# Kernel tuning notes

Measured on AMD Instinct MI355X. Metric: run time of the kernel, lower is better.

The kernel has to match this reference:

```python
import jax, jax.numpy as jnp
import numpy as np

B, IN, O, F, FH = 512, 2000, 64, 8, 32
D = 64 + FH * O  # 2112


def setup_inputs() -> dict:
    key = jax.random.key(0)
    ks = jax.random.split(key, 17)
    rn = lambda k, s: jax.random.normal(k, s, dtype=jnp.float32) * 0.05
    return dict(
        x=rn(ks[0], (B, IN)),
        fc_in_W=rn(ks[1], (1024, IN)), fc_in_b=rn(ks[2], (1024,)),
        fc1_W=rn(ks[3], (128, 1024)), fc1_b=rn(ks[4], (128,)),
        out1_W=rn(ks[5], (O, 64, 128)), out1_b=rn(ks[6], (O, 64)),
        coef_nn_W=rn(ks[7], (F, FH, 1)), coef_nn_b=rn(ks[8], (F, FH)),
        coef_att_W=rn(ks[9], (F, FH, FH)),
        out_att_W=rn(ks[10], (O, FH, FH)),
        nodes_trans_W=rn(ks[11], (O, O)),
        trans_gcn_W=rn(ks[12], (D, D)),
        outmap_W=rn(ks[13], (1, D)), outmap_b=rn(ks[14], (1,)),
        prelu_a=jnp.float32(0.25),
        coef_m=rn(ks[15], (O, O, F)),
    )


def reference(x, fc_in_W, fc_in_b, fc1_W, fc1_b, out1_W, out1_b,
              coef_nn_W, coef_nn_b, coef_att_W, out_att_W,
              nodes_trans_W, trans_gcn_W, outmap_W, outmap_b, prelu_a, coef_m):
    elu = jax.nn.elu
    # trunk MLP
    h = jax.nn.relu(x @ fc_in_W.T + fc_in_b)          # [B,1024]
    h = jax.nn.relu(h @ fc1_W.T + fc1_b)              # [B,128]
    # per-output-node heads (vectorized over the output_dim loop)
    hiddens = jax.nn.relu(jnp.einsum('bk,odk->bod', h, out1_W) + out1_b)  # [B,O,64]
    # per-feature coef embedding: Linear(1,FH) on each coef_m[:,:,i] slice
    cf = elu(coef_m[..., None] * coef_nn_W[:, :, 0] + coef_nn_b)          # [O,O,F,FH]
    # sum over concatenated feature axis (F*FH) of exp(elu(.))
    s = jnp.exp(elu(cf)).sum(axis=(2, 3))[:, :, None, None]               # [O,O,1,1]
    lin = jnp.einsum('xyfh,fgh->xyfg', cf, coef_att_W)                    # per-feature attention linear
    p = elu(jnp.exp(elu(cf)) * lin / s)
    cfs = elu(p.sum(axis=2) / F)                                          # [O,O,FH]
    # node-level attention (vectorized over the output_dim loop)
    coef_sum = jnp.exp(elu(cfs)).sum(axis=1)                              # [O,FH]
    p2 = jnp.exp(elu(cfs)) / coef_sum[:, None, :]                         # [O,O,FH]
    lin2 = jnp.einsum('oih,igh->oig', cfs, out_att_W)
    att = (p2 * lin2).reshape(O, O * FH)                                  # concat over i (i-major)
    hc = jnp.concatenate(
        [hiddens, jnp.broadcast_to(att[None], (x.shape[0], O, O * FH))], axis=2)  # [B,O,D]
    nt = jnp.einsum('bpd,op->bod', hc, nodes_trans_W)                     # node mixing Linear(O,O)
    trans = jax.nn.sigmoid(jnp.einsum('bod,ed->boe', nt, trans_gcn_W))    # [B,O,D]
    z = (trans @ outmap_W.T + outmap_b).squeeze(-1)                       # [B,O]
    return jnp.where(z >= 0, z, prelu_a * z)                              # PReLU
```

## Files before the change

kernel.cpp:

```cpp
#include <hip/hip_runtime.h>
#include <math.h>

typedef __attribute__((ext_vector_type(8))) short bf16x8;
typedef __attribute__((ext_vector_type(4))) float f32x4;

static __device__ __forceinline__ float fast_elu(float x) {
    return x > 0.0f ? x : __expf(x) - 1.0f;
}

static __device__ __forceinline__ unsigned short f2bf(float f) {
    unsigned int u = __float_as_uint(f);
    unsigned int r = (u + 0x7FFFu + ((u >> 16) & 1u)) >> 16;
    return (unsigned short)r;
}

#define CV0 1048576
#define CV1 3145728
#define CV2 3276800
#define CV3 3280896
#define CV4 3805184
#define CV5 8265728
__global__ __launch_bounds__(256) void conv_all(
    const float* __restrict__ x, const float* __restrict__ fcinW,
    const float* __restrict__ fc1W, const float* __restrict__ ntW,
    const float* __restrict__ out1W, const float* __restrict__ tgw,
    unsigned short* __restrict__ xb, unsigned short* __restrict__ fcinWb,
    unsigned short* __restrict__ fc1Wb, unsigned short* __restrict__ Wb,
    unsigned short* __restrict__ out1WbT,
    unsigned short* __restrict__ Gb, unsigned short* __restrict__ G2b)
{
    int idx = blockIdx.x * 256 + threadIdx.x;
    if (idx < CV0) {
        int r = idx >> 11, k = idx & 2047;
        xb[idx] = (k < 2000) ? f2bf(x[(size_t)r * 2000 + k]) : (unsigned short)0;
    } else if (idx < CV1) {
        int i = idx - CV0;
        int r = i >> 11, k = i & 2047;
        fcinWb[i] = (k < 2000) ? f2bf(fcinW[(size_t)r * 2000 + k]) : (unsigned short)0;
    } else if (idx < CV2) {
        int i = idx - CV1;
        fc1Wb[i] = f2bf(fc1W[i]);
    } else if (idx < CV3) {
        int i = idx - CV2;
        Wb[i] = f2bf(ntW[i]);
    } else if (idx < CV4) {
        int i = idx - CV3;
        int n = i >> 7, k = i & 127, d = n >> 6, p = n & 63;
        out1WbT[i] = f2bf(out1W[(size_t)((p << 6) | d) * 128 + k]);
    } else if (idx < CV5) {
        int i = idx - CV4;
        int e = i / 2112, k = i - e * 2112;
        unsigned short v = f2bf(tgw[(size_t)e * 2112 + k]);
        if (k < 64) Gb[e * 64 + k] = v;
        else        G2b[(size_t)e * 2048 + (k - 64)] = v;
    }
}

__global__ __launch_bounds__(256) void gemm_mfma(
    const unsigned short* __restrict__ A, int lda,
    const unsigned short* __restrict__ B, int ldb,
    float* __restrict__ C, unsigned short* __restrict__ Cb,
    int ldc, long strideCz,
    const float* __restrict__ bias, int mode, int kchunk)
{
    __shared__ __align__(16) unsigned short As[64 * 40];
    __shared__ __align__(16) unsigned short Bs[64 * 40];
    const int t = threadIdx.x;
    const int w = t >> 6, lane = t & 63, l16 = lane & 15, quad = lane >> 4;
    const int n0 = blockIdx.x * 64, m0 = blockIdx.y * 64;
    const int kb0 = blockIdx.z * kchunk;
    const int r = t >> 2, koff = (t & 3) * 8;
    if (mode == 0) C += (size_t)blockIdx.z * strideCz;

    const size_t arow = (size_t)(m0 + r) * lda + koff;
    const size_t brow = (size_t)(n0 + r) * ldb + koff;
    bf16x8 av = *reinterpret_cast<const bf16x8*>(&A[arow + kb0]);
    bf16x8 bv = *reinterpret_cast<const bf16x8*>(&B[brow + kb0]);

    f32x4 acc[4] = {};
    for (int kb = kb0; kb < kb0 + kchunk; kb += 32) {
        __syncthreads();
        *reinterpret_cast<bf16x8*>(&As[r * 40 + koff]) = av;
        *reinterpret_cast<bf16x8*>(&Bs[r * 40 + koff]) = bv;
        if (kb + 32 < kb0 + kchunk) {
            av = *reinterpret_cast<const bf16x8*>(&A[arow + kb + 32]);
            bv = *reinterpret_cast<const bf16x8*>(&B[brow + kb + 32]);
        }
        __syncthreads();
        bf16x8 af = *reinterpret_cast<const bf16x8*>(&As[(w * 16 + l16) * 40 + quad * 8]);
        #pragma unroll
        for (int nt = 0; nt < 4; ++nt) {
            bf16x8 bf = *reinterpret_cast<const bf16x8*>(&Bs[(nt * 16 + l16) * 40 + quad * 8]);
            acc[nt] = __builtin_amdgcn_mfma_f32_16x16x32_bf16(af, bf, acc[nt], 0, 0, 0);
        }
    }
    #pragma unroll
    for (int nt = 0; nt < 4; ++nt)
        #pragma unroll
        for (int i = 0; i < 4; ++i) {
            int m = m0 + w * 16 + quad * 4 + i;
            int n = n0 + nt * 16 + l16;
            if (mode == 0) {
                C[(size_t)m * ldc + n] = acc[nt][i];
            } else {
                int bidx = (((n & 63) << 6) | (n >> 6));
                float v = acc[nt][i] + bias[bidx];
                v = fmaxf(v, 0.0f);
                Cb[(size_t)m * ldc + n] = f2bf(v);
            }
        }
}

__global__ __launch_bounds__(256) void gemm_mfma_fa(
    const float* __restrict__ Ap, int lda, long apstride, int nparts,
    const float* __restrict__ abias,
    const unsigned short* __restrict__ B, int ldb,
    float* __restrict__ C, unsigned short* __restrict__ Cb,
    int ldc, long strideCz,
    const float* __restrict__ bias, int mode, int kchunk)
{
    __shared__ __align__(16) unsigned short As[64 * 40];
    __shared__ __align__(16) unsigned short Bs[64 * 40];
    const int t = threadIdx.x;
    const int w = t >> 6, lane = t & 63, l16 = lane & 15, quad = lane >> 4;
    const int n0 = blockIdx.x * 64, m0 = blockIdx.y * 64;
    const int kb0 = blockIdx.z * kchunk;
    const int r = t >> 2, koff = (t & 3) * 8;
    if (mode == 0) C += (size_t)blockIdx.z * strideCz;

    f32x4 acc[4] = {};
    for (int kb = kb0; kb < kb0 + kchunk; kb += 32) {
        float a8[8];
        {
            const float* base = &Ap[(size_t)(m0 + r) * lda + kb + koff];
            float4 s0 = *reinterpret_cast<const float4*>(base);
            float4 s1 = *reinterpret_cast<const float4*>(base + 4);
            for (int j = 1; j < nparts; ++j) {
                const float* pj = base + (size_t)j * apstride;
                float4 p0 = *reinterpret_cast<const float4*>(pj);
                float4 p1 = *reinterpret_cast<const float4*>(pj + 4);
                s0.x += p0.x; s0.y += p0.y; s0.z += p0.z; s0.w += p0.w;
                s1.x += p1.x; s1.y += p1.y; s1.z += p1.z; s1.w += p1.w;
            }
            float4 b0 = *reinterpret_cast<const float4*>(&abias[kb + koff]);
            float4 b1 = *reinterpret_cast<const float4*>(&abias[kb + koff + 4]);
            a8[0] = fmaxf(s0.x + b0.x, 0.0f); a8[1] = fmaxf(s0.y + b0.y, 0.0f);
            a8[2] = fmaxf(s0.z + b0.z, 0.0f); a8[3] = fmaxf(s0.w + b0.w, 0.0f);
            a8[4] = fmaxf(s1.x + b1.x, 0.0f); a8[5] = fmaxf(s1.y + b1.y, 0.0f);
            a8[6] = fmaxf(s1.z + b1.z, 0.0f); a8[7] = fmaxf(s1.w + b1.w, 0.0f);
        }
        bf16x8 bv = *reinterpret_cast<const bf16x8*>(&B[(size_t)(n0 + r) * ldb + kb + koff]);
        __syncthreads();
        ushort4 lo, hi;
        lo.x = f2bf(a8[0]); lo.y = f2bf(a8[1]); lo.z = f2bf(a8[2]); lo.w = f2bf(a8[3]);
        hi.x = f2bf(a8[4]); hi.y = f2bf(a8[5]); hi.z = f2bf(a8[6]); hi.w = f2bf(a8[7]);
        *reinterpret_cast<ushort4*>(&As[r * 40 + koff]) = lo;
        *reinterpret_cast<ushort4*>(&As[r * 40 + koff + 4]) = hi;
        *reinterpret_cast<bf16x8*>(&Bs[r * 40 + koff]) = bv;
        __syncthreads();
        bf16x8 af = *reinterpret_cast<const bf16x8*>(&As[(w * 16 + l16) * 40 + quad * 8]);
        #pragma unroll
        for (int nt = 0; nt < 4; ++nt) {
            bf16x8 bf = *reinterpret_cast<const bf16x8*>(&Bs[(nt * 16 + l16) * 40 + quad * 8]);
            acc[nt] = __builtin_amdgcn_mfma_f32_16x16x32_bf16(af, bf, acc[nt], 0, 0, 0);
        }
    }
    #pragma unroll
    for (int nt = 0; nt < 4; ++nt)
        #pragma unroll
        for (int i = 0; i < 4; ++i) {
            int m = m0 + w * 16 + quad * 4 + i;
            int n = n0 + nt * 16 + l16;
            if (mode == 0) {
                C[(size_t)m * ldc + n] = acc[nt][i];
            } else {
                int bidx = (((n & 63) << 6) | (n >> 6));
                float v = acc[nt][i] + bias[bidx];
                v = fmaxf(v, 0.0f);
                Cb[(size_t)m * ldc + n] = f2bf(v);
            }
        }
}

__global__ __launch_bounds__(256) void reduce_partials(
    const float* __restrict__ src, float* __restrict__ dst, int n,
    int nparts, long pstride)
{
    int i = blockIdx.x * 256 + threadIdx.x;
    if (i >= n) return;
    float a = 0.0f;
    for (int j = 0; j < nparts; ++j) a += src[i + (long)j * pstride];
    dst[i] = a;
}

__global__ __launch_bounds__(256) void coef_kernel(
    const float* __restrict__ coef_m,
    const float* __restrict__ cW,
    const float* __restrict__ cB,
    const float* __restrict__ attW,
    float* __restrict__ cfs)
{
    __shared__ float cf_s[4][256];
    __shared__ float part[4][64];
    const int t = threadIdx.x;
    const int wv = t >> 6, lane = t & 63;
    const int xy = blockIdx.x * 4 + wv;
    float ls = 0.0f;
    #pragma unroll
    for (int i = 0; i < 4; ++i) {
        int idx = i * 64 + lane;
        int f = idx >> 5;
        float v = fast_elu(coef_m[xy * 8 + f] * cW[idx] + cB[idx]);
        cf_s[wv][idx] = v;
        ls += __expf(fast_elu(v));
    }
    #pragma unroll
    for (int m = 1; m < 64; m <<= 1) ls += __shfl_xor(ls, m, 64);
    __syncthreads();
    const float rs = __builtin_amdgcn_rcpf(ls);
    const int g = lane & 31, fg = lane >> 5;
    float acc = 0.0f;
    for (int f = fg * 4; f < fg * 4 + 4; ++f) {
        float lin = 0.0f;
        #pragma unroll
        for (int h = 0; h < 32; h += 4) {
            float4 Lv = *reinterpret_cast<const float4*>(&cf_s[wv][f * 32 + h]);
            float4 Wv = *reinterpret_cast<const float4*>(&attW[f * 1024 + g * 32 + h]);
            lin += Lv.x * Wv.x + Lv.y * Wv.y + Lv.z * Wv.z + Lv.w * Wv.w;
        }
        float e = __expf(fast_elu(cf_s[wv][f * 32 + g]));
        acc += fast_elu(e * lin * rs);
    }
    part[wv][lane] = acc;
    __syncthreads();
    if (lane < 32) {
        float tot = part[wv][lane] + part[wv][lane + 32];
        cfs[xy * 32 + lane] = fast_elu(tot * 0.125f);
    }
}

__global__ __launch_bounds__(256) void att_split(
    const float* __restrict__ cfs,
    const float* __restrict__ oattW,
    float* __restrict__ att)
{
    __shared__ float L[2048];
    __shared__ float red[256];
    __shared__ float csum[32];
    const int t = threadIdx.x;
    const int o = blockIdx.x;
    const int ic = blockIdx.y;
    #pragma unroll
    for (int j = 0; j < 8; ++j) L[t + 256 * j] = cfs[o * 2048 + t + 256 * j];
    __syncthreads();
    {
        int h = t & 31, ig = t >> 5;
        float ps = 0.0f;
        for (int i = ig * 8; i < ig * 8 + 8; ++i) ps += __expf(fast_elu(L[i * 32 + h]));
        red[t] = ps;
        __syncthreads();
        if (t < 32) {
            float cs = 0.0f;
            #pragma unroll
            for (int j = 0; j < 8; ++j) cs += red[j * 32 + t];
            csum[t] = cs;
        }
        __syncthreads();
    }
    int idx = ic * 256 + t;
    int i = idx >> 5, g = idx & 31;
    float lin2 = 0.0f;
    #pragma unroll
    for (int h = 0; h < 32; h += 4) {
        float4 Lv = *reinterpret_cast<const float4*>(&L[i * 32 + h]);
        float4 Wv = *reinterpret_cast<const float4*>(&oattW[i * 1024 + g * 32 + h]);
        lin2 += Lv.x * Wv.x + Lv.y * Wv.y + Lv.z * Wv.z + Lv.w * Wv.w;
    }
    float p2 = __expf(fast_elu(L[idx])) * __builtin_amdgcn_rcpf(csum[g]);
    att[o * 2048 + idx] = p2 * lin2;
}

__global__ __launch_bounds__(256) void natt_new(
    const float* __restrict__ ntW,
    const float* __restrict__ att,
    unsigned short* __restrict__ nattb)
{
    __shared__ float ntW_s[64 * 65];
    __shared__ float att_s[64 * 17];
    const int t = threadIdx.x;
    const int d0 = blockIdx.x * 16;
    #pragma unroll
    for (int j = 0; j < 16; ++j) {
        int idx = t + 256 * j;
        ntW_s[(idx >> 6) * 65 + (idx & 63)] = ntW[idx];
    }
    #pragma unroll
    for (int j = 0; j < 4; ++j) {
        int idx = t + 256 * j;
        int p = idx >> 4, dd = idx & 15;
        att_s[p * 17 + dd] = att[p * 2048 + d0 + dd];
    }
    __syncthreads();
    const int dd = t & 15, ob = (t >> 4) * 4;
    float acc[4] = {0.0f, 0.0f, 0.0f, 0.0f};
    for (int p = 0; p < 64; ++p) {
        float av = att_s[p * 17 + dd];
        #pragma unroll
        for (int i = 0; i < 4; ++i) acc[i] += ntW_s[(ob + i) * 65 + p] * av;
    }
    #pragma unroll
    for (int i = 0; i < 4; ++i)
        nattb[(ob + i) * 2048 + d0 + dd] = f2bf(acc[i]);
}

__global__ __launch_bounds__(256) void nt1f(
    const unsigned short* __restrict__ hbT,
    const unsigned short* __restrict__ Wb,
    unsigned short* __restrict__ nt1b)
{
    __shared__ __align__(16) unsigned short HtT[64 * 72];
    __shared__ __align__(16) unsigned short nt1_s[64 * 72];
    const int t = threadIdx.x;
    const int w = t >> 6, lane = t & 63, l16 = lane & 15, quad = lane >> 4;
    const int b = blockIdx.x;

    const unsigned short* src = hbT + (size_t)b * 4096;
    #pragma unroll
    for (int j = 0; j < 2; ++j) {
        int c = t + j * 256;
        *reinterpret_cast<bf16x8*>(&HtT[(c >> 3) * 72 + (c & 7) * 8]) =
            *reinterpret_cast<const bf16x8*>(&src[c * 8]);
    }
    __syncthreads();

    bf16x8 aW[2];
    #pragma unroll
    for (int h = 0; h < 2; ++h)
        aW[h] = *reinterpret_cast<const bf16x8*>(&Wb[(w * 16 + l16) * 64 + h * 32 + quad * 8]);
    #pragma unroll
    for (int dt = 0; dt < 4; ++dt) {
        f32x4 acc = {0.0f, 0.0f, 0.0f, 0.0f};
        #pragma unroll
        for (int h = 0; h < 2; ++h) {
            bf16x8 bf = *reinterpret_cast<const bf16x8*>(
                &HtT[(dt * 16 + l16) * 72 + h * 32 + quad * 8]);
            acc = __builtin_amdgcn_mfma_f32_16x16x32_bf16(aW[h], bf, acc, 0, 0, 0);
        }
        #pragma unroll
        for (int i = 0; i < 4; ++i)
            nt1_s[(w * 16 + quad * 4 + i) * 72 + dt * 16 + l16] = f2bf(acc[i]);
    }
    __syncthreads();
    #pragma unroll
    for (int j = 0; j < 2; ++j) {
        int c = t + j * 256;
        *reinterpret_cast<bf16x8*>(&nt1b[(size_t)b * 4096 + c * 8]) =
            *reinterpret_cast<const bf16x8*>(&nt1_s[(c >> 3) * 72 + (c & 7) * 8]);
    }
}

__global__ __launch_bounds__(256) void final_eblk(
    const unsigned short* __restrict__ nt1b,
    const unsigned short* __restrict__ Gb,
    const float* __restrict__ cmatT,
    const float* __restrict__ outW,
    float* __restrict__ zpart)
{
    __shared__ __align__(16) unsigned short nls[2][64 * 72];
    __shared__ float zs[2][4][64];
    const int t = threadIdx.x;
    const int w = t >> 6, lane = t & 63, l16 = lane & 15, quad = lane >> 4;
    const int eb = blockIdx.x;
    const int b0 = blockIdx.y * 32;
    const int ew = eb * 64 + w * 16;

    bf16x8 ga[2];
    #pragma unroll
    for (int h = 0; h < 2; ++h)
        ga[h] = *reinterpret_cast<const bf16x8*>(
            &Gb[(size_t)(ew + l16) * 64 + h * 32 + quad * 8]);
    float cm[4][4];
    #pragma unroll
    for (int nt = 0; nt < 4; ++nt)
        #pragma unroll
        for (int i = 0; i < 4; ++i)
            cm[nt][i] = cmatT[(size_t)(ew + quad * 4 + i) * 64 + nt * 16 + l16];
    float wv[4];
    #pragma unroll
    for (int i = 0; i < 4; ++i) wv[i] = outW[ew + quad * 4 + i];

    const int c0 = t, c1 = t + 256;
    bf16x8 v0 = *reinterpret_cast<const bf16x8*>(&nt1b[(size_t)b0 * 4096 + c0 * 8]);
    bf16x8 v1 = *reinterpret_cast<const bf16x8*>(&nt1b[(size_t)b0 * 4096 + c1 * 8]);
    *reinterpret_cast<bf16x8*>(&nls[0][(c0 >> 3) * 72 + (c0 & 7) * 8]) = v0;
    *reinterpret_cast<bf16x8*>(&nls[0][(c1 >> 3) * 72 + (c1 & 7) * 8]) = v1;
    __syncthreads();

    int cur = 0;
    for (int bi = 0; bi < 32; ++bi) {
        if (bi < 31) {
            v0 = *reinterpret_cast<const bf16x8*>(
                &nt1b[(size_t)(b0 + bi + 1) * 4096 + c0 * 8]);
            v1 = *reinterpret_cast<const bf16x8*>(
                &nt1b[(size_t)(b0 + bi + 1) * 4096 + c1 * 8]);
        }
        if (bi > 0 && t < 64) {
            const float* z = &zs[(bi - 1) & 1][0][0];
            zpart[((size_t)eb * 512 + b0 + bi - 1) * 64 + t] =
                z[t] + z[64 + t] + z[128 + t] + z[192 + t];
        }
        float zo[4] = {0.0f, 0.0f, 0.0f, 0.0f};
        #pragma unroll
        for (int nt = 0; nt < 4; ++nt) {
            bf16x8 bf0 = *reinterpret_cast<const bf16x8*>(
                &nls[cur][(nt * 16 + l16) * 72 + quad * 8]);
            bf16x8 bf1 = *reinterpret_cast<const bf16x8*>(
                &nls[cur][(nt * 16 + l16) * 72 + 32 + quad * 8]);
            f32x4 acc = {cm[nt][0], cm[nt][1], cm[nt][2], cm[nt][3]};
            acc = __builtin_amdgcn_mfma_f32_16x16x32_bf16(ga[0], bf0, acc, 0, 0, 0);
            acc = __builtin_amdgcn_mfma_f32_16x16x32_bf16(ga[1], bf1, acc, 0, 0, 0);
            #pragma unroll
            for (int i = 0; i < 4; ++i)
                zo[nt] += __builtin_amdgcn_rcpf(1.0f + __expf(-acc[i])) * wv[i];
        }
        #pragma unroll
        for (int nt = 0; nt < 4; ++nt) {
            zo[nt] += __shfl_xor(zo[nt], 16, 64);
            zo[nt] += __shfl_xor(zo[nt], 32, 64);
        }
        if (quad == 0) {
            #pragma unroll
            for (int nt = 0; nt < 4; ++nt)
                zs[bi & 1][w][nt * 16 + l16] = zo[nt];
        }
        if (bi < 31) {
            *reinterpret_cast<bf16x8*>(&nls[1 - cur][(c0 >> 3) * 72 + (c0 & 7) * 8]) = v0;
            *reinterpret_cast<bf16x8*>(&nls[1 - cur][(c1 >> 3) * 72 + (c1 & 7) * 8]) = v1;
        }
        __syncthreads();
        cur ^= 1;
    }
    if (t < 64) {
        const float* z = &zs[1][0][0];
        zpart[((size_t)eb * 512 + b0 + 31) * 64 + t] =
            z[t] + z[64 + t] + z[128 + t] + z[192 + t];
    }
}

__global__ __launch_bounds__(256) void finish_kernel(
    const float* __restrict__ zpart, const float* __restrict__ outB,
    const float* __restrict__ preluA, float* __restrict__ out)
{
    int i = blockIdx.x * 256 + threadIdx.x;
    float z = 0.0f;
    for (int j = 0; j < 33; ++j) z += zpart[(size_t)j * 32768 + i];
    z += outB[0];
    float pa = preluA[0];
    out[i] = (z >= 0.0f) ? z : pa * z;
}

extern "C" void kernel_launch(void* const* d_in, const int* in_sizes, int n_in,
                              void* d_out, int out_size, void* d_ws, size_t ws_size,
                              hipStream_t stream)
{
    const float* x       = (const float*)d_in[0];
    const float* fc_in_W = (const float*)d_in[1];
    const float* fc_in_b = (const float*)d_in[2];
    const float* fc1_W   = (const float*)d_in[3];
    const float* fc1_b   = (const float*)d_in[4];
    const float* out1_W  = (const float*)d_in[5];
    const float* out1_b  = (const float*)d_in[6];
    const float* cW      = (const float*)d_in[7];
    const float* cB      = (const float*)d_in[8];
    const float* cattW   = (const float*)d_in[9];
    const float* oattW   = (const float*)d_in[10];
    const float* ntW     = (const float*)d_in[11];
    const float* tgw     = (const float*)d_in[12];
    const float* outW    = (const float*)d_in[13];
    const float* outB    = (const float*)d_in[14];
    const float* preluA  = (const float*)d_in[15];
    const float* coef_m  = (const float*)d_in[16];
    float* out = (float*)d_out;
    float* ws  = (float*)d_ws;

    unsigned short* xb      = (unsigned short*)(ws + 0);
    unsigned short* fcinWb  = (unsigned short*)(ws + 524288);
    float*          cpT     = ws + 0;
    float*          h1p     = ws + 1572864;
    unsigned short* nt1b    = (unsigned short*)(ws + 1572864);
    float*          zpart   = ws + 2621440;
    unsigned short* fc1Wb   = (unsigned short*)(ws + 3670016);
    float*          h2p     = ws + 3735552;
    unsigned short* out1WbT = (unsigned short*)(ws + 3997696);
    unsigned short* hbT     = (unsigned short*)(ws + 4259840);
    unsigned short* Wb      = (unsigned short*)(ws + 5308416);
    unsigned short* Gb      = (unsigned short*)(ws + 5310464);
    unsigned short* G2b     = (unsigned short*)(ws + 5378048);
    float*          att     = ws + 7540736;
    unsigned short* nattb   = (unsigned short*)(ws + 7671808);
    float*          cmatT   = ws + 7737344;
    float*          cfs     = ws + 7737344;

    conv_all<<<(CV5 + 255) / 256, 256, 0, stream>>>(
        x, fc_in_W, fc1_W, ntW, out1_W, tgw,
        xb, fcinWb, fc1Wb, Wb, out1WbT, Gb, G2b);

    coef_kernel<<<1024, 256, 0, stream>>>(coef_m, cW, cB, cattW, cfs);
    att_split<<<dim3(64, 8), 256, 0, stream>>>(cfs, oattW, att);
    natt_new<<<128, 256, 0, stream>>>(ntW, att, nattb);

    gemm_mfma<<<dim3(16, 8, 4), 256, 0, stream>>>(xb, 2048, fcinWb, 2048,
        h1p, nullptr, 1024, 524288L, nullptr, 0, 512);
    gemm_mfma_fa<<<dim3(2, 8, 4), 256, 0, stream>>>(h1p, 1024, 524288L, 4,
        fc_in_b, fc1Wb, 1024, h2p, nullptr, 128, 65536L, nullptr, 0, 256);
    gemm_mfma_fa<<<dim3(64, 8, 1), 256, 0, stream>>>(h2p, 128, 65536L, 4,
        fc1_b, out1WbT, 128, nullptr, hbT, 4096, 0L, out1_b, 2, 128);

    gemm_mfma<<<dim3(1, 33, 8), 256, 0, stream>>>(G2b, 2048, nattb, 2048,
        cpT, nullptr, 64, 135168L, nullptr, 0, 256);
    reduce_partials<<<528, 256, 0, stream>>>(cpT, cmatT, 135168, 8, 135168L);

    nt1f<<<512, 256, 0, stream>>>(hbT, Wb, nt1b);
    final_eblk<<<dim3(33, 16), 256, 0, stream>>>(nt1b, Gb, cmatT, outW, zpart);
    finish_kernel<<<128, 256, 0, stream>>>(zpart, outB, preluA, out);
}
```

Measured before the change: 227.4 us.

## Merge independent kernels into combined launches and split final kernel finer

Combines pairs of independent stages (conversion with coef, fc_in GEMM with attention, fc1 GEMM with node attention, head GEMM with cmat GEMM, nt1f with partial reduction) into shared launches that dispatch on block index. This cuts launch count and lets small side-branch work fill idle compute units alongside the main GEMMs. The final kernel processes 16 batch rows per block instead of 32, doubling the grid for better occupancy. The risk is larger shared memory per block in the combined kernels, and imbalanced block durations.

```diff
diff --git a/kernel.cpp b/kernel.cpp
--- a/kernel.cpp
+++ b/kernel.cpp
@@ -20,7 +20,10 @@
 #define CV3 3280896
 #define CV4 3805184
 #define CV5 8265728
-__global__ __launch_bounds__(256) void conv_all(
+#define CONV_BLOCKS 32288
+
+static __device__ __forceinline__ void conv_phase(
+    int bx,
     const float* __restrict__ x, const float* __restrict__ fcinW,
     const float* __restrict__ fc1W, const float* __restrict__ ntW,
     const float* __restrict__ out1W, const float* __restrict__ tgw,
@@ -29,7 +32,7 @@
     unsigned short* __restrict__ out1WbT,
     unsigned short* __restrict__ Gb, unsigned short* __restrict__ G2b)
 {
-    int idx = blockIdx.x * 256 + threadIdx.x;
+    int idx = bx * 256 + threadIdx.x;
     if (idx < CV0) {
         int r = idx >> 11, k = idx & 2047;
         xb[idx] = (k < 2000) ? f2bf(x[(size_t)r * 2000 + k]) : (unsigned short)0;
@@ -56,21 +59,137 @@
     }
 }
 
-__global__ __launch_bounds__(256) void gemm_mfma(
+static __device__ __forceinline__ void coef_phase(
+    int bx, float* __restrict__ smemf,
+    const float* __restrict__ coef_m, const float* __restrict__ cW,
+    const float* __restrict__ cB, const float* __restrict__ attW,
+    float* __restrict__ cfs)
+{
+    float* cf_s = smemf;
+    float* part = smemf + 1024;
+    const int t = threadIdx.x;
+    const int wv = t >> 6, lane = t & 63;
+    const int xy = bx * 4 + wv;
+    float ls = 0.0f;
+    #pragma unroll
+    for (int i = 0; i < 4; ++i) {
+        int idx = i * 64 + lane;
+        int f = idx >> 5;
+        float v = fast_elu(coef_m[xy * 8 + f] * cW[idx] + cB[idx]);
+        cf_s[wv * 256 + idx] = v;
+        ls += __expf(fast_elu(v));
+    }
+    #pragma unroll
+    for (int m = 1; m < 64; m <<= 1) ls += __shfl_xor(ls, m, 64);
+    __syncthreads();
+    const float rs = __builtin_amdgcn_rcpf(ls);
+    const int g = lane & 31, fg = lane >> 5;
+    float acc = 0.0f;
+    for (int f = fg * 4; f < fg * 4 + 4; ++f) {
+        float lin = 0.0f;
+        #pragma unroll
+        for (int h = 0; h < 32; h += 4) {
+            float4 Lv = *reinterpret_cast<const float4*>(&cf_s[wv * 256 + f * 32 + h]);
+            float4 Wv = *reinterpret_cast<const float4*>(&attW[f * 1024 + g * 32 + h]);
+            lin += Lv.x * Wv.x + Lv.y * Wv.y + Lv.z * Wv.z + Lv.w * Wv.w;
+        }
+        float e = __expf(fast_elu(cf_s[wv * 256 + f * 32 + g]));
+        acc += fast_elu(e * lin * rs);
+    }
+    part[wv * 64 + lane] = acc;
+    __syncthreads();
+    if (lane < 32) {
+        float tot = part[wv * 64 + lane] + part[wv * 64 + lane + 32];
+        cfs[xy * 32 + lane] = fast_elu(tot * 0.125f);
+    }
+}
+
+static __device__ __forceinline__ void att_phase(
+    int o, int ic, float* __restrict__ smemf,
+    const float* __restrict__ cfs, const float* __restrict__ oattW,
+    float* __restrict__ att)
+{
+    float* L    = smemf;
+    float* red  = smemf + 2048;
+    float* csum = smemf + 2304;
+    const int t = threadIdx.x;
+    #pragma unroll
+    for (int j = 0; j < 8; ++j) L[t + 256 * j] = cfs[o * 2048 + t + 256 * j];
+    __syncthreads();
+    {
+        int h = t & 31, ig = t >> 5;
+        float ps = 0.0f;
+        for (int i = ig * 8; i < ig * 8 + 8; ++i) ps += __expf(fast_elu(L[i * 32 + h]));
+        red[t] = ps;
+        __syncthreads();
+        if (t < 32) {
+            float cs = 0.0f;
+            #pragma unroll
+            for (int j = 0; j < 8; ++j) cs += red[j * 32 + t];
+            csum[t] = cs;
+        }
+        __syncthreads();
+    }
+    int idx = ic * 256 + t;
+    int i = idx >> 5, g = idx & 31;
+    float lin2 = 0.0f;
+    #pragma unroll
+    for (int h = 0; h < 32; h += 4) {
+        float4 Lv = *reinterpret_cast<const float4*>(&L[i * 32 + h]);
+        float4 Wv = *reinterpret_cast<const float4*>(&oattW[i * 1024 + g * 32 + h]);
+        lin2 += Lv.x * Wv.x + Lv.y * Wv.y + Lv.z * Wv.z + Lv.w * Wv.w;
+    }
+    float p2 = __expf(fast_elu(L[idx])) * __builtin_amdgcn_rcpf(csum[g]);
+    att[o * 2048 + idx] = p2 * lin2;
+}
+
+static __device__ __forceinline__ void natt_phase(
+    int bx, float* __restrict__ smemf,
+    const float* __restrict__ ntW, const float* __restrict__ att,
+    unsigned short* __restrict__ nattb)
+{
+    float* ntW_s = smemf;
+    float* att_s = smemf + 64 * 65;
+    const int t = threadIdx.x;
+    const int d0 = bx * 16;
+    #pragma unroll
+    for (int j = 0; j < 16; ++j) {
+        int idx = t + 256 * j;
+        ntW_s[(idx >> 6) * 65 + (idx & 63)] = ntW[idx];
+    }
+    #pragma unroll
+    for (int j = 0; j < 4; ++j) {
+        int idx = t + 256 * j;
+        int p = idx >> 4, dd = idx & 15;
+        att_s[p * 17 + dd] = att[p * 2048 + d0 + dd];
+    }
+    __syncthreads();
+    const int dd = t & 15, ob = (t >> 4) * 4;
+    float acc[4] = {0.0f, 0.0f, 0.0f, 0.0f};
+    for (int p = 0; p < 64; ++p) {
+        float av = att_s[p * 17 + dd];
+        #pragma unroll
+        for (int i = 0; i < 4; ++i) acc[i] += ntW_s[(ob + i) * 65 + p] * av;
+    }
+    #pragma unroll
+    for (int i = 0; i < 4; ++i)
+        nattb[(ob + i) * 2048 + d0 + dd] = f2bf(acc[i]);
+}
+
+static __device__ __forceinline__ void gemm_core(
     const unsigned short* __restrict__ A, int lda,
     const unsigned short* __restrict__ B, int ldb,
     float* __restrict__ C, unsigned short* __restrict__ Cb,
-    int ldc, long strideCz,
-    const float* __restrict__ bias, int mode, int kchunk)
-{
-    __shared__ __align__(16) unsigned short As[64 * 40];
-    __shared__ __align__(16) unsigned short Bs[64 * 40];
+    int ldc, long strideCz, const float* __restrict__ bias,
+    int mode, int kchunk, int bn, int bm, int bz,
+    unsigned short* __restrict__ As, unsigned short* __restrict__ Bs)
+{
     const int t = threadIdx.x;
     const int w = t >> 6, lane = t & 63, l16 = lane & 15, quad = lane >> 4;
-    const int n0 = blockIdx.x * 64, m0 = blockIdx.y * 64;
-    const int kb0 = blockIdx.z * kchunk;
+    const int n0 = bn * 64, m0 = bm * 64;
+    const int kb0 = bz * kchunk;
     const int r = t >> 2, koff = (t & 3) * 8;
-    if (mode == 0) C += (size_t)blockIdx.z * strideCz;
+    if (mode == 0) C += (size_t)bz * strideCz;
 
     const size_t arow = (size_t)(m0 + r) * lda + koff;
     const size_t brow = (size_t)(n0 + r) * ldb + koff;
@@ -111,22 +230,21 @@
         }
 }
 
-__global__ __launch_bounds__(256) void gemm_mfma_fa(
+static __device__ __forceinline__ void gemm_fa_core(
     const float* __restrict__ Ap, int lda, long apstride, int nparts,
     const float* __restrict__ abias,
     const unsigned short* __restrict__ B, int ldb,
     float* __restrict__ C, unsigned short* __restrict__ Cb,
-    int ldc, long strideCz,
-    const float* __restrict__ bias, int mode, int kchunk)
-{
-    __shared__ __align__(16) unsigned short As[64 * 40];
-    __shared__ __align__(16) unsigned short Bs[64 * 40];
+    int ldc, long strideCz, const float* __restrict__ bias,
+    int mode, int kchunk, int bn, int bm, int bz,
+    unsigned short* __restrict__ As, unsigned short* __restrict__ Bs)
+{
     const int t = threadIdx.x;
     const int w = t >> 6, lane = t & 63, l16 = lane & 15, quad = lane >> 4;
-    const int n0 = blockIdx.x * 64, m0 = blockIdx.y * 64;
-    const int kb0 = blockIdx.z * kchunk;
+    const int n0 = bn * 64, m0 = bm * 64;
+    const int kb0 = bz * kchunk;
     const int r = t >> 2, koff = (t & 3) * 8;
-    if (mode == 0) C += (size_t)blockIdx.z * strideCz;
+    if (mode == 0) C += (size_t)bz * strideCz;
 
     f32x4 acc[4] = {};
     for (int kb = kb0; kb < kb0 + kchunk; kb += 32) {
@@ -182,147 +300,15 @@
         }
 }
 
-__global__ __launch_bounds__(256) void reduce_partials(
-    const float* __restrict__ src, float* __restrict__ dst, int n,
-    int nparts, long pstride)
-{
-    int i = blockIdx.x * 256 + threadIdx.x;
-    if (i >= n) return;
-    float a = 0.0f;
-    for (int j = 0; j < nparts; ++j) a += src[i + (long)j * pstride];
-    dst[i] = a;
-}
-
-__global__ __launch_bounds__(256) void coef_kernel(
-    const float* __restrict__ coef_m,
-    const float* __restrict__ cW,
-    const float* __restrict__ cB,
-    const float* __restrict__ attW,
-    float* __restrict__ cfs)
-{
-    __shared__ float cf_s[4][256];
-    __shared__ float part[4][64];
-    const int t = threadIdx.x;
-    const int wv = t >> 6, lane = t & 63;
-    const int xy = blockIdx.x * 4 + wv;
-    float ls = 0.0f;
-    #pragma unroll
-    for (int i = 0; i < 4; ++i) {
-        int idx = i * 64 + lane;
-        int f = idx >> 5;
-        float v = fast_elu(coef_m[xy * 8 + f] * cW[idx] + cB[idx]);
-        cf_s[wv][idx] = v;
-        ls += __expf(fast_elu(v));
-    }
-    #pragma unroll
-    for (int m = 1; m < 64; m <<= 1) ls += __shfl_xor(ls, m, 64);
-    __syncthreads();
-    const float rs = __builtin_amdgcn_rcpf(ls);
-    const int g = lane & 31, fg = lane >> 5;
-    float acc = 0.0f;
-    for (int f = fg * 4; f < fg * 4 + 4; ++f) {
-        float lin = 0.0f;
-        #pragma unroll
-        for (int h = 0; h < 32; h += 4) {
-            float4 Lv = *reinterpret_cast<const float4*>(&cf_s[wv][f * 32 + h]);
-            float4 Wv = *reinterpret_cast<const float4*>(&attW[f * 1024 + g * 32 + h]);
-            lin += Lv.x * Wv.x + Lv.y * Wv.y + Lv.z * Wv.z + Lv.w * Wv.w;
-        }
-        float e = __expf(fast_elu(cf_s[wv][f * 32 + g]));
-        acc += fast_elu(e * lin * rs);
-    }
-    part[wv][lane] = acc;
-    __syncthreads();
-    if (lane < 32) {
-        float tot = part[wv][lane] + part[wv][lane + 32];
-        cfs[xy * 32 + lane] = fast_elu(tot * 0.125f);
-    }
-}
-
-__global__ __launch_bounds__(256) void att_split(
-    const float* __restrict__ cfs,
-    const float* __restrict__ oattW,
-    float* __restrict__ att)
-{
-    __shared__ float L[2048];
-    __shared__ float red[256];
-    __shared__ float csum[32];
-    const int t = threadIdx.x;
-    const int o = blockIdx.x;
-    const int ic = blockIdx.y;
-    #pragma unroll
-    for (int j = 0; j < 8; ++j) L[t + 256 * j] = cfs[o * 2048 + t + 256 * j];
-    __syncthreads();
-    {
-        int h = t & 31, ig = t >> 5;
-        float ps = 0.0f;
-        for (int i = ig * 8; i < ig * 8 + 8; ++i) ps += __expf(fast_elu(L[i * 32 + h]));
-        red[t] = ps;
-        __syncthreads();
-        if (t < 32) {
-            float cs = 0.0f;
-            #pragma unroll
-            for (int j = 0; j < 8; ++j) cs += red[j * 32 + t];
-            csum[t] = cs;
-        }
-        __syncthreads();
-    }
-    int idx = ic * 256 + t;
-    int i = idx >> 5, g = idx & 31;
-    float lin2 = 0.0f;
-    #pragma unroll
-    for (int h = 0; h < 32; h += 4) {
-        float4 Lv = *reinterpret_cast<const float4*>(&L[i * 32 + h]);
-        float4 Wv = *reinterpret_cast<const float4*>(&oattW[i * 1024 + g * 32 + h]);
-        lin2 += Lv.x * Wv.x + Lv.y * Wv.y + Lv.z * Wv.z + Lv.w * Wv.w;
-    }
-    float p2 = __expf(fast_elu(L[idx])) * __builtin_amdgcn_rcpf(csum[g]);
-    att[o * 2048 + idx] = p2 * lin2;
-}
-
-__global__ __launch_bounds__(256) void natt_new(
-    const float* __restrict__ ntW,
-    const float* __restrict__ att,
-    unsigned short* __restrict__ nattb)
-{
-    __shared__ float ntW_s[64 * 65];
-    __shared__ float att_s[64 * 17];
-    const int t = threadIdx.x;
-    const int d0 = blockIdx.x * 16;
-    #pragma unroll
-    for (int j = 0; j < 16; ++j) {
-        int idx = t + 256 * j;
-        ntW_s[(idx >> 6) * 65 + (idx & 63)] = ntW[idx];
-    }
-    #pragma unroll
-    for (int j = 0; j < 4; ++j) {
-        int idx = t + 256 * j;
-        int p = idx >> 4, dd = idx & 15;
-        att_s[p * 17 + dd] = att[p * 2048 + d0 + dd];
-    }
-    __syncthreads();
-    const int dd = t & 15, ob = (t >> 4) * 4;
-    float acc[4] = {0.0f, 0.0f, 0.0f, 0.0f};
-    for (int p = 0; p < 64; ++p) {
-        float av = att_s[p * 17 + dd];
-        #pragma unroll
-        for (int i = 0; i < 4; ++i) acc[i] += ntW_s[(ob + i) * 65 + p] * av;
-    }
-    #pragma unroll
-    for (int i = 0; i < 4; ++i)
-        nattb[(ob + i) * 2048 + d0 + dd] = f2bf(acc[i]);
-}
-
-__global__ __launch_bounds__(256) void nt1f(
-    const unsigned short* __restrict__ hbT,
-    const unsigned short* __restrict__ Wb,
+static __device__ __forceinline__ void nt1f_phase(
+    int b, unsigned short* __restrict__ smemu,
+    const unsigned short* __restrict__ hbT, const unsigned short* __restrict__ Wb,
     unsigned short* __restrict__ nt1b)
 {
-    __shared__ __align__(16) unsigned short HtT[64 * 72];
-    __shared__ __align__(16) unsigned short nt1_s[64 * 72];
+    unsigned short* HtT   = smemu;
+    unsigned short* nt1_s = smemu + 64 * 72;
     const int t = threadIdx.x;
     const int w = t >> 6, lane = t & 63, l16 = lane & 15, quad = lane >> 4;
-    const int b = blockIdx.x;
 
     const unsigned short* src = hbT + (size_t)b * 4096;
     #pragma unroll
@@ -356,6 +342,95 @@
         int c = t + j * 256;
         *reinterpret_cast<bf16x8*>(&nt1b[(size_t)b * 4096 + c * 8]) =
             *reinterpret_cast<const bf16x8*>(&nt1_s[(c >> 3) * 72 + (c & 7) * 8]);
+    }
+}
+
+__global__ __launch_bounds__(256) void uber1(
+    const float* x, const float* fcinW, const float* fc1W, const float* ntW,
+    const float* out1W, const float* tgw,
+    unsigned short* xb, unsigned short* fcinWb, unsigned short* fc1Wb,
+    unsigned short* Wb, unsigned short* out1WbT,
+    unsigned short* Gb, unsigned short* G2b,
+    const float* coef_m, const float* cW, const float* cB, const float* attW,
+    float* cfs)
+{
+    __shared__ __align__(16) float smemf[1280];
+    int bx = blockIdx.x;
+    if (bx < CONV_BLOCKS)
+        conv_phase(bx, x, fcinW, fc1W, ntW, out1W, tgw,
+                   xb, fcinWb, fc1Wb, Wb, out1WbT, Gb, G2b);
+    else
+        coef_phase(bx - CONV_BLOCKS, smemf, coef_m, cW, cB, attW, cfs);
+}
+
+__global__ __launch_bounds__(256) void uber2(
+    const unsigned short* xb, const unsigned short* fcinWb, float* h1p,
+    const float* cfs, const float* oattW, float* att)
+{
+    __shared__ __align__(16) float smemf[2592];
+    int bx = blockIdx.x;
+    if (bx < 512) {
+        unsigned short* As = (unsigned short*)smemf;
+        gemm_core(xb, 2048, fcinWb, 2048, h1p, nullptr, 1024, 524288L,
+                  nullptr, 0, 512, bx & 15, (bx >> 4) & 7, bx >> 7, As, As + 2560);
+    } else {
+        int b2 = bx - 512;
+        att_phase(b2 & 63, b2 >> 6, smemf, cfs, oattW, att);
+    }
+}
+
+__global__ __launch_bounds__(256) void uber3(
+    const float* h1p, const float* fc_in_b, const unsigned short* fc1Wb,
+    float* h2p,
+    const float* ntW, const float* att, unsigned short* nattb)
+{
+    __shared__ __align__(16) float smemf[5248];
+    int bx = blockIdx.x;
+    if (bx < 64) {
+        unsigned short* As = (unsigned short*)smemf;
+        gemm_fa_core(h1p, 1024, 524288L, 4, fc_in_b, fc1Wb, 1024,
+                     h2p, nullptr, 128, 65536L, nullptr, 0, 256,
+                     bx & 1, (bx >> 1) & 7, bx >> 4, As, As + 2560);
+    } else {
+        natt_phase(bx - 64, smemf, ntW, att, nattb);
+    }
+}
+
+__global__ __launch_bounds__(256) void uber4(
+    const float* h2p, const float* fc1_b, const unsigned short* out1WbT,
+    unsigned short* hbT, const float* out1_b,
+    const unsigned short* G2b, const unsigned short* nattb, float* cpT)
+{
+    __shared__ __align__(16) float smemf[2560];
+    unsigned short* As = (unsigned short*)smemf;
+    int bx = blockIdx.x;
+    if (bx < 512) {
+        gemm_fa_core(h2p, 128, 65536L, 4, fc1_b, out1WbT, 128,
+                     nullptr, hbT, 4096, 0L, out1_b, 2, 128,
+                     bx & 63, bx >> 6, 0, As, As + 2560);
+    } else {
+        int b2 = bx - 512;
+        gemm_core(G2b, 2048, nattb, 2048, cpT, nullptr, 64, 135168L,
+                  nullptr, 0, 256, 0, b2 % 33, b2 / 33, As, As + 2560);
+    }
+}
+
+__global__ __launch_bounds__(256) void uber5(
+    const unsigned short* hbT, const unsigned short* Wb, unsigned short* nt1b,
+    const float* cpT, float* cmatT)
+{
+    __shared__ __align__(16) unsigned short smemu[2 * 64 * 72];
+    int bx = blockIdx.x;
+    if (bx < 512) {
+        nt1f_phase(bx, smemu, hbT, Wb, nt1b);
+    } else {
+        int i = (bx - 512) * 256 + threadIdx.x;
+        if (i < 135168) {
+            float a = 0.0f;
+            #pragma unroll
+            for (int j = 0; j < 8; ++j) a += cpT[i + (long)j * 135168L];
+            cmatT[i] = a;
+        }
     }
 }
 
@@ -371,7 +446,7 @@
     const int t = threadIdx.x;
     const int w = t >> 6, lane = t & 63, l16 = lane & 15, quad = lane >> 4;
     const int eb = blockIdx.x;
-    const int b0 = blockIdx.y * 32;
+    const int b0 = blockIdx.y * 16;
     const int ew = eb * 64 + w * 16;
 
     bf16x8 ga[2];
@@ -397,8 +472,8 @@
     __syncthreads();
 
     int cur = 0;
-    for (int bi = 0; bi < 32; ++bi) {
-        if (bi < 31) {
+    for (int bi = 0; bi < 16; ++bi) {
+        if (bi < 15) {
             v0 = *reinterpret_cast<const bf16x8*>(
                 &nt1b[(size_t)(b0 + bi + 1) * 4096 + c0 * 8]);
             v1 = *reinterpret_cast<const bf16x8*>(
@@ -433,7 +508,7 @@
             for (int nt = 0; nt < 4; ++nt)
                 zs[bi & 1][w][nt * 16 + l16] = zo[nt];
         }
-        if (bi < 31) {
+        if (bi < 15) {
             *reinterpret_cast<bf16x8*>(&nls[1 - cur][(c0 >> 3) * 72 + (c0 & 7) * 8]) = v0;
             *reinterpret_cast<bf16x8*>(&nls[1 - cur][(c1 >> 3) * 72 + (c1 & 7) * 8]) = v1;
         }
@@ -442,7 +517,7 @@
     }
     if (t < 64) {
         const float* z = &zs[1][0][0];
-        zpart[((size_t)eb * 512 + b0 + 31) * 64 + t] =
+        zpart[((size_t)eb * 512 + b0 + 15) * 64 + t] =
             z[t] + z[64 + t] + z[128 + t] + z[192 + t];
     }
 }
@@ -501,26 +576,15 @@
     float*          cmatT   = ws + 7737344;
     float*          cfs     = ws + 7737344;
 
-    conv_all<<<(CV5 + 255) / 256, 256, 0, stream>>>(
+    uber1<<<CONV_BLOCKS + 1024, 256, 0, stream>>>(
         x, fc_in_W, fc1_W, ntW, out1_W, tgw,
-        xb, fcinWb, fc1Wb, Wb, out1WbT, Gb, G2b);
-
-    coef_kernel<<<1024, 256, 0, stream>>>(coef_m, cW, cB, cattW, cfs);
-    att_split<<<dim3(64, 8), 256, 0, stream>>>(cfs, oattW, att);
-    natt_new<<<128, 256, 0, stream>>>(ntW, att, nattb);
-
-    gemm_mfma<<<dim3(16, 8, 4), 256, 0, stream>>>(xb, 2048, fcinWb, 2048,
-        h1p, nullptr, 1024, 524288L, nullptr, 0, 512);
-    gemm_mfma_fa<<<dim3(2, 8, 4), 256, 0, stream>>>(h1p, 1024, 524288L, 4,
-        fc_in_b, fc1Wb, 1024, h2p, nullptr, 128, 65536L, nullptr, 0, 256);
-    gemm_mfma_fa<<<dim3(64, 8, 1), 256, 0, stream>>>(h2p, 128, 65536L, 4,
-        fc1_b, out1WbT, 128, nullptr, hbT, 4096, 0L, out1_b, 2, 128);
-
-    gemm_mfma<<<dim3(1, 33, 8), 256, 0, stream>>>(G2b, 2048, nattb, 2048,
-        cpT, nullptr, 64, 135168L, nullptr, 0, 256);
-    reduce_partials<<<528, 256, 0, stream>>>(cpT, cmatT, 135168, 8, 135168L);
-
-    nt1f<<<512, 256, 0, stream>>>(hbT, Wb, nt1b);
-    final_eblk<<<dim3(33, 16), 256, 0, stream>>>(nt1b, Gb, cmatT, outW, zpart);
+        xb, fcinWb, fc1Wb, Wb, out1WbT, Gb, G2b,
+        coef_m, cW, cB, cattW, cfs);
+    uber2<<<1024, 256, 0, stream>>>(xb, fcinWb, h1p, cfs, oattW, att);
+    uber3<<<192, 256, 0, stream>>>(h1p, fc_in_b, fc1Wb, h2p, ntW, att, nattb);
+    uber4<<<776, 256, 0, stream>>>(h2p, fc1_b, out1WbT, hbT, out1_b,
+                                   G2b, nattb, cpT);
+    uber5<<<1040, 256, 0, stream>>>(hbT, Wb, nt1b, cpT, cmatT);
+    final_eblk<<<dim3(33, 32), 256, 0, stream>>>(nt1b, Gb, cmatT, outW, zpart);
     finish_kernel<<<128, 256, 0, stream>>>(zpart, outB, preluA, out);
 }
```

Result: faster. 201.1 us (-11.6%).
